# Performance work log

Measured on AMD Instinct MI355X. Metric: run time of the kernel, lower is better.

## Reference

```python
import jax, jax.numpy as jnp
import numpy as np

EMBED_DIM = 1024
NUM_HEADS = 16
HEAD_DIM = EMBED_DIM // NUM_HEADS
SEQ = 2048
BSZ = 4


def setup_inputs() -> dict:
    key = jax.random.key(0)
    k1, k2, k3 = jax.random.split(key, 3)
    x = jax.random.normal(k1, (SEQ, BSZ, EMBED_DIM), dtype=jnp.float32)
    # xavier-uniform-like init for projection weights
    lim_in = float(np.sqrt(6.0 / (EMBED_DIM + 3 * EMBED_DIM)))
    lim_out = float(np.sqrt(6.0 / (EMBED_DIM + EMBED_DIM)))
    W_in = jax.random.uniform(k2, (3 * EMBED_DIM, EMBED_DIM), minval=-lim_in, maxval=lim_in, dtype=jnp.float32)
    b_in = jnp.zeros((3 * EMBED_DIM,), dtype=jnp.float32)
    W_out = jax.random.uniform(k3, (EMBED_DIM, EMBED_DIM), minval=-lim_out, maxval=lim_out, dtype=jnp.float32)
    b_out = jnp.zeros((EMBED_DIM,), dtype=jnp.float32)
    return {"x": x, "W_in": W_in, "b_in": b_in, "W_out": W_out, "b_out": b_out}


def reference(x, W_in, b_in, W_out, b_out):
    # x: [S, B, E] (seq-first, as in the torch module)
    S, B, E = x.shape
    H, D = NUM_HEADS, HEAD_DIM
    qkv = jnp.einsum('sbe,fe->sbf', x, W_in) + b_in          # [S, B, 3E]
    q, k, v = jnp.split(qkv, 3, axis=-1)
    # [S, B, E] -> [B, H, S, D]
    q = q.reshape(S, B, H, D).transpose(1, 2, 0, 3)
    k = k.reshape(S, B, H, D).transpose(1, 2, 0, 3)
    v = v.reshape(S, B, H, D).transpose(1, 2, 0, 3)
    scale = 1.0 / jnp.sqrt(jnp.asarray(D, dtype=x.dtype))
    scores = jnp.einsum('bhsd,bhtd->bhst', q, k) * scale      # [B, H, S, S]
    attn = jax.nn.softmax(scores, axis=-1)                    # dropout p=0.0 -> identity
    out = jnp.einsum('bhst,bhtd->bhsd', attn, v)              # [B, H, S, D]
    out = out.transpose(2, 0, 1, 3).reshape(S, B, E)          # [S, B, E]
    out = jnp.einsum('sbe,fe->sbf', out, W_out) + b_out
    return out, attn
```

## Files before the change

kernel.cpp:

```cpp
#include <hip/hip_runtime.h>
#include <stdint.h>

#define SEQ 2048
#define BSZ 4
#define EMB 1024
#define NH  16
#define HD  64
#define BH  (BSZ*NH)
#define MROWS (SEQ*BSZ)

typedef __attribute__((ext_vector_type(8))) short short8;
typedef __attribute__((ext_vector_type(4))) float f32x4;
typedef __attribute__((ext_vector_type(4))) unsigned short us4;

__device__ __forceinline__ unsigned short f2bf(float f) {
  unsigned u = __float_as_uint(f);
  u += 0x7fffu + ((u >> 16) & 1u);
  return (unsigned short)(u >> 16);
}

#define GLDS(g, l) __builtin_amdgcn_global_load_lds( \
    (const __attribute__((address_space(1))) void*)(g), \
    (__attribute__((address_space(3))) void*)(l), 16, 0, 0)

__global__ void k_cvt(const float* __restrict__ in, unsigned short* __restrict__ out, int n4) {
  int i = blockIdx.x * blockDim.x + threadIdx.x;
  int stride = gridDim.x * blockDim.x;
  for (; i < n4; i += stride) {
    float4 v = reinterpret_cast<const float4*>(in)[i];
    us4 o;
    o[0] = f2bf(v.x); o[1] = f2bf(v.y); o[2] = f2bf(v.z); o[3] = f2bf(v.w);
    reinterpret_cast<us4*>(out)[i] = o;
  }
}

template<int MODE>
__global__ __launch_bounds__(256, 2) void k_gemm_bt(
    const unsigned short* __restrict__ A, const unsigned short* __restrict__ B,
    const float* __restrict__ bias, float* __restrict__ outF,
    unsigned short* __restrict__ qb, unsigned short* __restrict__ kb,
    unsigned short* __restrict__ vb, int M, int N, int K)
{
  __shared__ unsigned short As[128*32];
  __shared__ unsigned short Bs[128*32];
  const int tid  = threadIdx.x;
  const int lane = tid & 63;
  const int wid  = tid >> 6;
  const int wr = wid >> 1, wc = wid & 1;
  const int r0 = blockIdx.y * 128;
  const int c0 = blockIdx.x * 128;
  const int lr = lane & 15;
  const int hi = lane >> 4;

  f32x4 acc[4][4];
  #pragma unroll
  for (int i = 0; i < 4; i++)
    #pragma unroll
    for (int j = 0; j < 4; j++) acc[i][j] = f32x4{0.f,0.f,0.f,0.f};

  const int nk = K >> 5;
  for (int kt = 0; kt < nk; ++kt) {
    #pragma unroll
    for (int j = 0; j < 2; ++j) {
      int e = (wid*2 + j)*512 + lane*8;
      int row = e >> 5, kk = e & 31;
      GLDS(A + (size_t)(r0 + row)*K + kt*32 + kk, &As[(wid*2+j)*512]);
      GLDS(B + (size_t)(c0 + row)*K + kt*32 + kk, &Bs[(wid*2+j)*512]);
    }
    __syncthreads();
    short8 af[4], bf[4];
    #pragma unroll
    for (int i = 0; i < 4; i++) af[i] = *(const short8*)&As[(wr*64 + i*16 + lr)*32 + hi*8];
    #pragma unroll
    for (int j = 0; j < 4; j++) bf[j] = *(const short8*)&Bs[(wc*64 + j*16 + lr)*32 + hi*8];
    #pragma unroll
    for (int i = 0; i < 4; i++)
      #pragma unroll
      for (int j = 0; j < 4; j++)
        acc[i][j] = __builtin_amdgcn_mfma_f32_16x16x32_bf16(af[i], bf[j], acc[i][j], 0, 0, 0);
    __syncthreads();
  }

  #pragma unroll
  for (int i = 0; i < 4; i++) {
    #pragma unroll
    for (int j = 0; j < 4; j++) {
      #pragma unroll
      for (int r = 0; r < 4; r++) {
        int row = r0 + wr*64 + i*16 + hi*4 + r;
        int col = c0 + wc*64 + j*16 + lr;
        float v = acc[i][j][r] + bias[col];
        if (MODE == 0) {
          outF[(size_t)row*N + col] = v;
        } else {
          int s = row >> 2, b = row & 3;
          int which = col >> 10, h = (col >> 6) & 15, d = col & 63;
          unsigned short bvv = f2bf(v);
          unsigned short* dst = (which == 0) ? qb : (which == 1) ? kb : vb;
          dst[((size_t)(b*NH + h)*SEQ + s)*HD + d] = bvv;
        }
      }
    }
  }
}

__global__ void k_transposeV(const unsigned short* __restrict__ V, unsigned short* __restrict__ Vt) {
  __shared__ unsigned short T[64][65];
  const int bh = blockIdx.y;
  const int s0 = blockIdx.x * 64;
  const int t = threadIdx.x;
  const int e = t * 16;
  {
    const int s = e >> 6, d0 = e & 63;
    short8 v0 = *(const short8*)&V[((size_t)bh*SEQ + s0 + s)*HD + d0];
    short8 v1 = *(const short8*)&V[((size_t)bh*SEQ + s0 + s)*HD + d0 + 8];
    #pragma unroll
    for (int q = 0; q < 8; q++) { T[s][d0+q] = (unsigned short)v0[q]; T[s][d0+8+q] = (unsigned short)v1[q]; }
  }
  __syncthreads();
  {
    const int d = e >> 6, sl = e & 63;
    short8 w0, w1;
    #pragma unroll
    for (int q = 0; q < 8; q++) { w0[q] = (short)T[sl+q][d]; w1[q] = (short)T[sl+8+q][d]; }
    *(short8*)&Vt[((size_t)bh*HD + d)*SEQ + s0 + sl]     = w0;
    *(short8*)&Vt[((size_t)bh*HD + d)*SEQ + s0 + sl + 8] = w1;
  }
}

__global__ __launch_bounds__(512, 4) void k_attn5(
    const unsigned short* __restrict__ Q, const unsigned short* __restrict__ Kb,
    const unsigned short* __restrict__ Vt, float* __restrict__ P,
    unsigned short* __restrict__ ctx)
{
  __shared__ unsigned short Ks[3][4096];
  __shared__ unsigned short Vs[3][4096];
  __shared__ float Pf[8][1024];

  const int i   = blockIdx.x;
  const int bh  = i & 63;
  const int rb  = i >> 6;

  const int tid = threadIdx.x;
  const int lane = tid & 63, w = tid >> 6;
  const int lr = lane & 15, hi = lane >> 4;
  const int q0 = rb * 128 + w * 16;
  const size_t qkBase = (size_t)bh * SEQ * HD;
  const size_t vtBase = (size_t)bh * HD * SEQ;

  const int srow = tid >> 3;
  const int scol = ((((tid & 7) * 16) ^ ((srow & 7) << 4)) >> 1);
  const int swz  = (lr & 7) << 4;

  #define STG_K(buf, kt) GLDS(Kb + qkBase + (size_t)((kt)*64 + srow)*HD + scol, \
                              (unsigned short*)Ks[buf] + tid*8)
  #define STG_V(buf, kt) GLDS(Vt + vtBase + (size_t)srow*SEQ + (kt)*64 + scol, \
                              (unsigned short*)Vs[buf] + tid*8)
  #define WAITV(n) asm volatile("s_waitcnt vmcnt(" #n ")" ::: "memory")
  #define BARRIER __builtin_amdgcn_s_barrier(); asm volatile("" ::: "memory")

  short8 bq0 = *(const short8*)&Q[qkBase + (size_t)(q0 + lr)*HD + hi*8];
  short8 bq1 = *(const short8*)&Q[qkBase + (size_t)(q0 + lr)*HD + 32 + hi*8];

  STG_K(0, 0); STG_K(1, 1);
  WAITV(1);
  BARRIER;
  float lsum = 0.f;
  {
    int cur = 0;
    for (int kt = 0; kt < 32; ++kt) {
      const char* kbase = (const char*)Ks[cur];
      #pragma unroll
      for (int ct = 0; ct < 4; ++ct) {
        const int rowb = (ct*16 + lr) * 128;
        short8 ak0 = *(const short8*)(kbase + ((rowb + hi*16) ^ swz));
        short8 ak1 = *(const short8*)(kbase + ((rowb + 64 + hi*16) ^ swz));
        f32x4 z = f32x4{0.f,0.f,0.f,0.f};
        z = __builtin_amdgcn_mfma_f32_16x16x32_bf16(ak0, bq0, z, 0, 0, 0);
        z = __builtin_amdgcn_mfma_f32_16x16x32_bf16(ak1, bq1, z, 0, 0, 0);
        lsum += __expf(z[0]*0.125f) + __expf(z[1]*0.125f)
              + __expf(z[2]*0.125f) + __expf(z[3]*0.125f);
      }
      int bs = cur + 2; if (bs >= 3) bs -= 3;
      if (kt < 30) {
        STG_K(bs, kt + 2);
        WAITV(1);
      } else {
        WAITV(0);
      }
      BARRIER;
      cur = (cur >= 2) ? 0 : cur + 1;
    }
  }
  float lv = lsum;
  lv += __shfl_xor(lv, 16);
  lv += __shfl_xor(lv, 32);
  const float li = 1.0f / lv;

  f32x4 o[4];
  #pragma unroll
  for (int d = 0; d < 4; ++d) o[d] = f32x4{0.f,0.f,0.f,0.f};

  float* pout = P + ((size_t)bh*SEQ + q0)*SEQ;
  char* pfw = (char*)Pf[w];

  STG_K(0, 0); STG_V(0, 0); STG_K(1, 1); STG_V(1, 1);
  WAITV(2);
  BARRIER;
  {
    int cur = 0;
    for (int kt = 0; kt < 32; ++kt) {
      const char* kbase = (const char*)Ks[cur];
      const char* vbase = (const char*)Vs[cur];
      #pragma unroll
      for (int ct = 0; ct < 4; ++ct) {
        const int rowb = (ct*16 + lr) * 128;
        short8 ak0 = *(const short8*)(kbase + ((rowb + hi*16) ^ swz));
        short8 ak1 = *(const short8*)(kbase + ((rowb + 64 + hi*16) ^ swz));
        f32x4 z = f32x4{0.f,0.f,0.f,0.f};
        z = __builtin_amdgcn_mfma_f32_16x16x32_bf16(ak0, bq0, z, 0, 0, 0);
        z = __builtin_amdgcn_mfma_f32_16x16x32_bf16(ak1, bq1, z, 0, 0, 0);
        f32x4 e;
        #pragma unroll
        for (int r = 0; r < 4; r++) e[r] = __expf(z[r]*0.125f) * li;
        *(f32x4*)(pfw + ((((ct*4 + hi) ^ lr) << 4) + lr*256)) = e;
      }
      #pragma unroll
      for (int j = 0; j < 4; ++j) {
        const int row = j*4 + hi;
        f32x4 pv4 = *(const f32x4*)(pfw + (row*256 + ((lr ^ row) << 4)));
        __builtin_nontemporal_store(pv4,
            (f32x4*)&pout[(size_t)row*SEQ + kt*64 + lr*4]);
      }
      #pragma unroll
      for (int s = 0; s < 2; ++s) {
        const int c0 = s*8 + hi*2;
        f32x4 f0 = *(const f32x4*)(pfw + (lr*256 + (((c0    ) ^ lr) << 4)));
        f32x4 f1 = *(const f32x4*)(pfw + (lr*256 + (((c0 + 1) ^ lr) << 4)));
        short8 pa;
        #pragma unroll
        for (int r = 0; r < 4; r++) { pa[r] = (short)f2bf(f0[r]); pa[4+r] = (short)f2bf(f1[r]); }
        #pragma unroll
        for (int dt = 0; dt < 4; ++dt) {
          const int rowb = (dt*16 + lr) * 128;
          short8 vb = *(const short8*)(vbase + ((rowb + s*64 + hi*16) ^ swz));
          o[dt] = __builtin_amdgcn_mfma_f32_16x16x32_bf16(pa, vb, o[dt], 0, 0, 0);
        }
      }
      if (kt < 30) {
        int bs = cur + 2; if (bs >= 3) bs -= 3;
        STG_K(bs, kt + 2); STG_V(bs, kt + 2);
        WAITV(6);
        BARRIER;
      } else if (kt == 30) {
        WAITV(4);
        BARRIER;
      }
      cur = (cur >= 2) ? 0 : cur + 1;
    }
  }

  const int b = bh >> 4, h = bh & 15;
  #pragma unroll
  for (int dt = 0; dt < 4; ++dt)
    #pragma unroll
    for (int r = 0; r < 4; r++) {
      int s = q0 + hi*4 + r;
      ctx[((size_t)s*BSZ + b)*EMB + h*HD + dt*16 + lr] = f2bf(o[dt][r]);
    }
  #undef STG_K
  #undef STG_V
  #undef WAITV
  #undef BARRIER
}

extern "C" void kernel_launch(void* const* d_in, const int* in_sizes, int n_in,
                              void* d_out, int out_size, void* d_ws, size_t ws_size,
                              hipStream_t stream) {
  const float* x     = (const float*)d_in[0];
  const float* W_in  = (const float*)d_in[1];
  const float* b_in  = (const float*)d_in[2];
  const float* W_out = (const float*)d_in[3];
  const float* b_out = (const float*)d_in[4];
  float* out   = (float*)d_out;
  float* attnP = out + (size_t)MROWS*EMB;

  char* ws = (char*)d_ws;
  size_t off = 0;
  auto alloc = [&](size_t bytes) { char* p = ws + off; off += (bytes + 255) & ~255ULL; return p; };
  unsigned short* Xbf    = (unsigned short*)alloc((size_t)MROWS*EMB*2);
  unsigned short* Winbf  = (unsigned short*)alloc((size_t)3*EMB*EMB*2);
  unsigned short* Woutbf = (unsigned short*)alloc((size_t)EMB*EMB*2);
  unsigned short* Qb  = (unsigned short*)alloc((size_t)BH*SEQ*HD*2);
  unsigned short* Kbf = (unsigned short*)alloc((size_t)BH*SEQ*HD*2);
  unsigned short* Vb  = (unsigned short*)alloc((size_t)BH*SEQ*HD*2);
  unsigned short* Vt  = (unsigned short*)alloc((size_t)BH*SEQ*HD*2);
  unsigned short* ctx = Xbf;

  k_cvt<<<2048, 256, 0, stream>>>(x,     Xbf,    MROWS*EMB/4);
  k_cvt<<<1024, 256, 0, stream>>>(W_in,  Winbf,  3*EMB*EMB/4);
  k_cvt<<<512,  256, 0, stream>>>(W_out, Woutbf, EMB*EMB/4);

  k_gemm_bt<1><<<dim3(3*EMB/128, MROWS/128), 256, 0, stream>>>(
      Xbf, Winbf, b_in, nullptr, Qb, Kbf, Vb, MROWS, 3*EMB, EMB);

  k_transposeV<<<dim3(SEQ/64, BH), 256, 0, stream>>>(Vb, Vt);

  k_attn5<<<1024, 512, 0, stream>>>(Qb, Kbf, Vt, attnP, ctx);

  k_gemm_bt<0><<<dim3(EMB/128, MROWS/128), 256, 0, stream>>>(
      ctx, Woutbf, b_out, out, nullptr, nullptr, nullptr, MROWS, EMB, EMB);
}
```

Measured before the change: 369.0 us.

## Merge cast kernels, swizzle GEMM block order, write V transposed from GEMM epilogue

The three fp32-to-bf16 conversion launches become one kernel that walks all three buffers. The GEMM remaps block IDs with an XCD-style swizzle so neighbouring tiles share L2. The QKV epilogue now writes V directly in [bh, d, s] layout, which removes the separate transpose kernel and its intermediate buffer. The V stores become strided 2-byte scatters, which may coalesce poorly compared with the old row-major writes.

```diff
diff --git a/kernel.cpp b/kernel.cpp
--- a/kernel.cpp
+++ b/kernel.cpp
@@ -23,14 +23,21 @@
     (const __attribute__((address_space(1))) void*)(g), \
     (__attribute__((address_space(3))) void*)(l), 16, 0, 0)
 
-__global__ void k_cvt(const float* __restrict__ in, unsigned short* __restrict__ out, int n4) {
+__global__ void k_cvt3(const float* __restrict__ x, const float* __restrict__ wi,
+                       const float* __restrict__ wo, unsigned short* __restrict__ xb,
+                       unsigned short* __restrict__ wib, unsigned short* __restrict__ wob) {
+  const int n0 = MROWS*EMB/4, n1 = 3*EMB*EMB/4, n2 = EMB*EMB/4;
   int i = blockIdx.x * blockDim.x + threadIdx.x;
-  int stride = gridDim.x * blockDim.x;
-  for (; i < n4; i += stride) {
-    float4 v = reinterpret_cast<const float4*>(in)[i];
+  const int stride = gridDim.x * blockDim.x;
+  for (; i < n0+n1+n2; i += stride) {
+    const float* src; unsigned short* dst; int j;
+    if (i < n0)           { src = x;  dst = xb;  j = i; }
+    else if (i < n0+n1)   { src = wi; dst = wib; j = i - n0; }
+    else                  { src = wo; dst = wob; j = i - n0 - n1; }
+    float4 v = reinterpret_cast<const float4*>(src)[j];
     us4 o;
     o[0] = f2bf(v.x); o[1] = f2bf(v.y); o[2] = f2bf(v.z); o[3] = f2bf(v.w);
-    reinterpret_cast<us4*>(out)[i] = o;
+    reinterpret_cast<us4*>(dst)[j] = o;
   }
 }
 
@@ -47,8 +54,14 @@
   const int lane = tid & 63;
   const int wid  = tid >> 6;
   const int wr = wid >> 1, wc = wid & 1;
-  const int r0 = blockIdx.y * 128;
-  const int c0 = blockIdx.x * 128;
+
+  const int fid = blockIdx.y * gridDim.x + blockIdx.x;
+  const int cpx = (gridDim.x * gridDim.y) >> 3;
+  const int swb = (fid & 7) * cpx + (fid >> 3);
+  const int bx = swb % gridDim.x, by = swb / gridDim.x;
+
+  const int r0 = by * 128;
+  const int c0 = bx * 128;
   const int lr = lane & 15;
   const int hi = lane >> 4;
 
@@ -96,35 +109,12 @@
           int s = row >> 2, b = row & 3;
           int which = col >> 10, h = (col >> 6) & 15, d = col & 63;
           unsigned short bvv = f2bf(v);
-          unsigned short* dst = (which == 0) ? qb : (which == 1) ? kb : vb;
-          dst[((size_t)(b*NH + h)*SEQ + s)*HD + d] = bvv;
+          if (which == 0)      qb[((size_t)(b*NH + h)*SEQ + s)*HD + d] = bvv;
+          else if (which == 1) kb[((size_t)(b*NH + h)*SEQ + s)*HD + d] = bvv;
+          else                 vb[((size_t)(b*NH + h)*HD + d)*SEQ + s] = bvv;
         }
       }
     }
-  }
-}
-
-__global__ void k_transposeV(const unsigned short* __restrict__ V, unsigned short* __restrict__ Vt) {
-  __shared__ unsigned short T[64][65];
-  const int bh = blockIdx.y;
-  const int s0 = blockIdx.x * 64;
-  const int t = threadIdx.x;
-  const int e = t * 16;
-  {
-    const int s = e >> 6, d0 = e & 63;
-    short8 v0 = *(const short8*)&V[((size_t)bh*SEQ + s0 + s)*HD + d0];
-    short8 v1 = *(const short8*)&V[((size_t)bh*SEQ + s0 + s)*HD + d0 + 8];
-    #pragma unroll
-    for (int q = 0; q < 8; q++) { T[s][d0+q] = (unsigned short)v0[q]; T[s][d0+8+q] = (unsigned short)v1[q]; }
-  }
-  __syncthreads();
-  {
-    const int d = e >> 6, sl = e & 63;
-    short8 w0, w1;
-    #pragma unroll
-    for (int q = 0; q < 8; q++) { w0[q] = (short)T[sl+q][d]; w1[q] = (short)T[sl+8+q][d]; }
-    *(short8*)&Vt[((size_t)bh*HD + d)*SEQ + s0 + sl]     = w0;
-    *(short8*)&Vt[((size_t)bh*HD + d)*SEQ + s0 + sl + 8] = w1;
   }
 }
 
@@ -293,18 +283,13 @@
   unsigned short* Woutbf = (unsigned short*)alloc((size_t)EMB*EMB*2);
   unsigned short* Qb  = (unsigned short*)alloc((size_t)BH*SEQ*HD*2);
   unsigned short* Kbf = (unsigned short*)alloc((size_t)BH*SEQ*HD*2);
-  unsigned short* Vb  = (unsigned short*)alloc((size_t)BH*SEQ*HD*2);
   unsigned short* Vt  = (unsigned short*)alloc((size_t)BH*SEQ*HD*2);
   unsigned short* ctx = Xbf;
 
-  k_cvt<<<2048, 256, 0, stream>>>(x,     Xbf,    MROWS*EMB/4);
-  k_cvt<<<1024, 256, 0, stream>>>(W_in,  Winbf,  3*EMB*EMB/4);
-  k_cvt<<<512,  256, 0, stream>>>(W_out, Woutbf, EMB*EMB/4);
+  k_cvt3<<<2048, 256, 0, stream>>>(x, W_in, W_out, Xbf, Winbf, Woutbf);
 
   k_gemm_bt<1><<<dim3(3*EMB/128, MROWS/128), 256, 0, stream>>>(
-      Xbf, Winbf, b_in, nullptr, Qb, Kbf, Vb, MROWS, 3*EMB, EMB);
-
-  k_transposeV<<<dim3(SEQ/64, BH), 256, 0, stream>>>(Vb, Vt);
+      Xbf, Winbf, b_in, nullptr, Qb, Kbf, Vt, MROWS, 3*EMB, EMB);
 
   k_attn5<<<1024, 512, 0, stream>>>(Qb, Kbf, Vt, attnP, ctx);
 
```

Result: no change. 374.9 us (+1.6%).
